# Optimization experiments

Hardware: AMD Instinct MI355X
Metric: run time of the kernel (lower is better)

The kernel has to match this reference:

```python
import jax, jax.numpy as jnp
import numpy as np

N, G, S = 51200, 512, 100   # nodes, graphs, nodes per graph
E = 512000                   # edges (within-graph)
F, H, D = 64, 4, 64
HD = H * D                   # 256
C = 10
RATIO = 0.8
NEG = -1e30


def _seg_softmax(logits, seg, mask, num_seg):
    # masked softmax over edges grouped by destination node
    lg = jnp.where(mask[:, None], logits, NEG)
    m = jax.lax.stop_gradient(jax.ops.segment_max(lg, seg, num_segments=num_seg))
    ex = jnp.where(mask[:, None], jnp.exp(lg - m[seg]), 0.0)
    s = jax.ops.segment_sum(ex, seg, num_segments=num_seg)
    return ex / jnp.maximum(s[seg], 1e-16)


def _gat_conv(x, src, dst, nmask, emask, W, att, b, Wres):
    # PyG GATConv: heads=4, concat=True, add_self_loops=True, residual Linear
    h = (x @ W).reshape(N, H, D)
    a_src = (h * att[0]).sum(-1)   # [N,H]
    a_dst = (h * att[1]).sum(-1)
    loop = jnp.arange(N, dtype=src.dtype)
    s2 = jnp.concatenate([src, loop])
    d2 = jnp.concatenate([dst, loop])
    em2 = jnp.concatenate([emask, nmask])
    logits = jax.nn.leaky_relu(a_src[s2] + a_dst[d2], 0.2)   # [E+N,H]
    alpha = _seg_softmax(logits, d2, em2, N)
    out = jax.ops.segment_sum(h[s2] * alpha[:, :, None], d2, num_segments=N)
    out = out.reshape(N, HD) + x @ Wres + b
    return out * nmask[:, None]


def _gt_conv(x, src, dst, nmask, emask, Wqkv, bqkv, Wskip, bskip):
    # PyG TransformerConv: heads=4, concat=True, root_weight=True (lin_skip)
    qkv = (x @ Wqkv + bqkv).reshape(N, 3, H, D)
    q, k, v = qkv[:, 0], qkv[:, 1], qkv[:, 2]
    logits = (q[dst] * k[src]).sum(-1) * (1.0 / np.sqrt(D))   # [E,H]
    alpha = _seg_softmax(logits, dst, emask, N)
    out = jax.ops.segment_sum(v[src] * alpha[:, :, None], dst, num_segments=N)
    return (out.reshape(N, HD) + x @ Wskip + bskip) * nmask[:, None]


def _topk_pool(x, w, batch, nmask, emask, src, dst):
    # PyG TopKPooling: score=tanh(x.w/|w|), keep top ceil(0.8*n) per graph,
    # x <- x*score, drop edges touching removed nodes. Masked (static-shape) form.
    score = jnp.tanh((x @ w) / jnp.linalg.norm(w))
    keyv = jnp.where(nmask, score, NEG)
    # composite key: sort by graph id, then by score descending (dead nodes last)
    ck = batch.astype(jnp.float32) * 4.0 - jnp.clip(keyv, -1.5, 1.5)
    order = jnp.argsort(ck)
    n_alive = jax.ops.segment_sum(nmask.astype(jnp.int32), batch, num_segments=G)
    k = jnp.ceil(RATIO * n_alive.astype(jnp.float32)).astype(jnp.int32)
    counts = jax.ops.segment_sum(jnp.ones(N, jnp.int32), batch, num_segments=G)
    start = jnp.cumsum(counts) - counts
    gs = batch[order]
    rank = jnp.arange(N, dtype=jnp.int32) - start[gs]
    keep = jnp.zeros(N, bool).at[order].set(rank < k[gs]) & nmask
    x_new = jnp.where(keep[:, None], x * score[:, None], 0.0)
    emask_new = emask & keep[src] & keep[dst]
    return x_new, keep, emask_new


def _readout(x, batch, nmask):
    # torch_geometric gmp || gap over alive nodes
    mx = jax.ops.segment_max(jnp.where(nmask[:, None], x, NEG), batch, num_segments=G)
    sm = jax.ops.segment_sum(x * nmask[:, None].astype(x.dtype), batch, num_segments=G)
    cnt = jax.ops.segment_sum(nmask.astype(x.dtype), batch, num_segments=G)
    return jnp.concatenate([mx, sm / jnp.maximum(cnt, 1.0)[:, None]], axis=1)


def _branch(x, src, dst, batch, conv, layers, pool_w):
    nmask = jnp.ones(N, bool)
    emask = jnp.ones(E, bool)
    acc = jnp.zeros((G, 2 * HD), x.dtype)
    for i in range(3):
        x = jax.nn.relu(conv(x, src, dst, nmask, emask, *layers[i]))
        x, nmask, emask = _topk_pool(x, pool_w[i], batch, nmask, emask, src, dst)
        acc = acc + _readout(x, batch, nmask)
    return acc


def _forward(x, edge_index, batch, gat1_W, gat1_att, gat1_b, gat1_res, gat2_W, gat2_att, gat2_b, gat2_res, gat3_W, gat3_att, gat3_b, gat3_res, gat_pool_w, gt1_Wqkv, gt1_bqkv, gt1_Wskip, gt1_bskip, gt2_Wqkv, gt2_bqkv, gt2_Wskip, gt2_bskip, gt3_Wqkv, gt3_bqkv, gt3_Wskip, gt3_bskip, gt_pool_w, lin1_W, lin1_b, lin2_W, lin2_b, lin3_W, lin3_b):
    src, dst = edge_index[0], edge_index[1]
    gat_layers = [(gat1_W, gat1_att, gat1_b, gat1_res),
                  (gat2_W, gat2_att, gat2_b, gat2_res),
                  (gat3_W, gat3_att, gat3_b, gat3_res)]
    gt_layers = [(gt1_Wqkv, gt1_bqkv, gt1_Wskip, gt1_bskip),
                 (gt2_Wqkv, gt2_bqkv, gt2_Wskip, gt2_bskip),
                 (gt3_Wqkv, gt3_bqkv, gt3_Wskip, gt3_bskip)]
    h1 = _branch(x, src, dst, batch, _gat_conv, gat_layers, gat_pool_w)
    h2 = _branch(x, src, dst, batch, _gt_conv, gt_layers, gt_pool_w)
    h = jnp.concatenate([h1, h2], axis=1)   # [G, 1024]
    h = jax.nn.relu(h @ lin1_W + lin1_b)
    # dropout p=0.5 skipped (eval mode)
    h = jax.nn.relu(h @ lin2_W + lin2_b)
    return jax.nn.log_softmax(h @ lin3_W + lin3_b, axis=-1)


def setup_inputs():
    keys = iter(jax.random.split(jax.random.key(0), 64))
    def nrm(shape, scale):
        return jax.random.normal(next(keys), shape, jnp.float32) * scale
    inp = {}
    inp["x"] = nrm((N, F), 1.0)
    src = jax.random.randint(next(keys), (E,), 0, N, jnp.int32)
    off = jax.random.randint(next(keys), (E,), 0, S, jnp.int32)
    dst = (src // S) * S + off   # keep edges within the source node's graph
    inp["edge_index"] = jnp.stack([src, dst])
    inp["batch"] = jnp.arange(N, dtype=jnp.int32) // S
    ins = [F, HD, HD]
    for i in range(3):
        fi = ins[i]
        sc = 1.0 / np.sqrt(fi)
        inp[f"gat{i+1}_W"] = nrm((fi, HD), sc)
        inp[f"gat{i+1}_att"] = nrm((2, H, D), 0.1)
        inp[f"gat{i+1}_b"] = jnp.zeros((HD,), jnp.float32)
        inp[f"gat{i+1}_res"] = nrm((fi, HD), sc)
        inp[f"gt{i+1}_Wqkv"] = nrm((fi, 3 * HD), sc)
        inp[f"gt{i+1}_bqkv"] = jnp.zeros((3 * HD,), jnp.float32)
        inp[f"gt{i+1}_Wskip"] = nrm((fi, HD), sc)
        inp[f"gt{i+1}_bskip"] = jnp.zeros((HD,), jnp.float32)
    inp["gat_pool_w"] = nrm((3, HD), 0.1)
    inp["gt_pool_w"] = nrm((3, HD), 0.1)
    inp["lin1_W"] = nrm((4 * HD, 128), 1.0 / np.sqrt(4 * HD))
    inp["lin1_b"] = jnp.zeros((128,), jnp.float32)
    inp["lin2_W"] = nrm((128, 64), 1.0 / np.sqrt(128.0))
    inp["lin2_b"] = jnp.zeros((64,), jnp.float32)
    inp["lin3_W"] = nrm((64, C), 1.0 / np.sqrt(64.0))
    inp["lin3_b"] = jnp.zeros((C,), jnp.float32)
    return inp


def reference(x, edge_index, batch, gat1_W, gat1_att, gat1_b, gat1_res, gat2_W, gat2_att, gat2_b, gat2_res, gat3_W, gat3_att, gat3_b, gat3_res, gat_pool_w, gt1_Wqkv, gt1_bqkv, gt1_Wskip, gt1_bskip, gt2_Wqkv, gt2_bqkv, gt2_Wskip, gt2_bskip, gt3_Wqkv, gt3_bqkv, gt3_Wskip, gt3_bskip, gt_pool_w, lin1_W, lin1_b, lin2_W, lin2_b, lin3_W, lin3_b):
    return _forward(x, edge_index, batch, gat1_W, gat1_att, gat1_b, gat1_res, gat2_W, gat2_att, gat2_b, gat2_res, gat3_W, gat3_att, gat3_b, gat3_res, gat_pool_w, gt1_Wqkv, gt1_bqkv, gt1_Wskip, gt1_bskip, gt2_Wqkv, gt2_bqkv, gt2_Wskip, gt2_bskip, gt3_Wqkv, gt3_bqkv, gt3_Wskip, gt3_bskip, gt_pool_w, lin1_W, lin1_b, lin2_W, lin2_b, lin3_W, lin3_b)
```

## Files before the change

kernel.cpp:

```cpp
#include <hip/hip_runtime.h>
#include <hip/hip_bf16.h>
#include <math.h>

#define N_NODES 51200
#define N_GRAPHS 512
#define S_NODES 100
#define N_EDGES 512000
#define HDF 256
#define NEGF (-1e30f)
#define DCAP 128

typedef short bf16x8 __attribute__((ext_vector_type(8)));
typedef float f32x4 __attribute__((ext_vector_type(4)));

__device__ inline unsigned short f2b(float x) {
    union { float f; unsigned u; } v; v.f = x;
    unsigned r = v.u + 0x7FFFu + ((v.u >> 16) & 1u);
    return (unsigned short)(r >> 16);
}
__device__ inline float b2f(unsigned short b) {
    union { float f; unsigned u; } v; v.u = ((unsigned)b) << 16; return v.f;
}

__global__ void set_int(int* __restrict__ p, int v, int n) {
    int i = blockIdx.x * 256 + threadIdx.x;
    if (i < n) p[i] = v;
}

__global__ void init_zero(int* __restrict__ deg, int* __restrict__ cursor,
                          float* __restrict__ acc1, float* __restrict__ acc2) {
    int i = blockIdx.x * 256 + threadIdx.x;
    if (i < N_NODES) { deg[i] = 0; cursor[i] = 0; }
    acc1[i] = 0.f;
    acc2[i] = 0.f;
}

struct WSplitDesc { const float* W; unsigned short* Wh; unsigned short* Wl; int K, NC; };
struct WSplitPack { WSplitDesc d[12]; };
__global__ void wsplit_all(WSplitPack p) {
    WSplitDesc d = p.d[blockIdx.y];
    int idx = blockIdx.x * 256 + threadIdx.x;
    if (idx >= d.K * d.NC) return;
    int k = idx / d.NC, c = idx - k * d.NC;
    float v = d.W[idx];
    unsigned short h = f2b(v);
    int o = ((k >> 3) * d.NC + c) * 8 + (k & 7);
    d.Wh[o] = h;
    d.Wl[o] = f2b(v - b2f(h));
}

__global__ __launch_bounds__(512) void mfma_gemm(
    const float* __restrict__ A,
    const unsigned short* __restrict__ Bh_g, const unsigned short* __restrict__ Bl_g,
    const float* __restrict__ bias, float* __restrict__ C,
    int K, int NC,
    const float* __restrict__ agg, int aggStride,
    const int* __restrict__ nmaskArr,
    const float* __restrict__ rowScale, const int* __restrict__ rsMask)
{
    __shared__ unsigned short Ah[4 * 128 * 8];
    __shared__ unsigned short Al[4 * 128 * 8];
    int row0 = blockIdx.y * 128, col0 = blockIdx.x * 256;
    int t = threadIdx.x;
    int lane = t & 63, w = t >> 6;
    int wr = w >> 2, wc = w & 3;
    int l15 = lane & 15, l4 = lane >> 4;
    f32x4 acc[4][4];
    #pragma unroll
    for (int m = 0; m < 4; ++m)
        #pragma unroll
        for (int n = 0; n < 4; ++n) acc[m][n] = (f32x4){0.f, 0.f, 0.f, 0.f};

    int arow = t & 127, akg = t >> 7;
    float ascale = 1.f;
    if (rowScale) ascale = rsMask[row0 + arow] ? rowScale[row0 + arow] : 0.f;

    for (int k0 = 0; k0 < K; k0 += 32) {
        const float* ap = A + (size_t)(row0 + arow) * K + k0 + akg * 8;
        float4 a0 = *(const float4*)ap;
        float4 a1 = *(const float4*)(ap + 4);
        float av[8] = {a0.x, a0.y, a0.z, a0.w, a1.x, a1.y, a1.z, a1.w};
        int abase = (akg * 128 + arow) * 8;
        #pragma unroll
        for (int j = 0; j < 8; ++j) {
            float s = av[j] * ascale;
            unsigned short h = f2b(s);
            Ah[abase + j] = h;
            Al[abase + j] = f2b(s - b2f(h));
        }
        __syncthreads();
        bf16x8 bh[4], bl[4];
        size_t brow = (size_t)((k0 >> 3) + l4) * NC;
        #pragma unroll
        for (int n = 0; n < 4; ++n) {
            size_t gb = (brow + col0 + wc * 64 + n * 16 + l15) * 8;
            bh[n] = *(const bf16x8*)&Bh_g[gb];
            bl[n] = *(const bf16x8*)&Bl_g[gb];
        }
        #pragma unroll
        for (int m = 0; m < 4; ++m) {
            int idx = (l4 * 128 + wr * 64 + m * 16 + l15) * 8;
            bf16x8 ah = *(bf16x8*)&Ah[idx];
            bf16x8 al = *(bf16x8*)&Al[idx];
            #pragma unroll
            for (int n = 0; n < 4; ++n) {
                acc[m][n] = __builtin_amdgcn_mfma_f32_16x16x32_bf16(ah, bh[n], acc[m][n], 0, 0, 0);
                acc[m][n] = __builtin_amdgcn_mfma_f32_16x16x32_bf16(ah, bl[n], acc[m][n], 0, 0, 0);
                acc[m][n] = __builtin_amdgcn_mfma_f32_16x16x32_bf16(al, bh[n], acc[m][n], 0, 0, 0);
            }
        }
        __syncthreads();
    }
    bool fused = (agg != nullptr);
    #pragma unroll
    for (int m = 0; m < 4; ++m) {
        #pragma unroll
        for (int n = 0; n < 4; ++n) {
            int col = col0 + wc * 64 + n * 16 + l15;
            float bv = bias ? bias[col] : 0.f;
            #pragma unroll
            for (int r = 0; r < 4; ++r) {
                int row = row0 + wr * 64 + m * 16 + l4 * 4 + r;
                float v = acc[m][n][r] + bv;
                if (fused) {
                    v += agg[(size_t)row * aggStride + col];
                    float nm = nmaskArr[row] ? 1.f : 0.f;
                    C[(size_t)row * 256 + col] = fmaxf(v, 0.f) * nm;
                } else {
                    C[(size_t)row * NC + col] = v;
                }
            }
        }
    }
}

__global__ void count_deg(const int* __restrict__ dst, int* __restrict__ deg) {
    int e = blockIdx.x * 256 + threadIdx.x;
    atomicAdd(&deg[dst[e]], 1);
}

__global__ __launch_bounds__(1024) void scan_deg(const int* __restrict__ deg,
                                                 int* __restrict__ rowStart) {
    __shared__ int part[1024];
    int t = threadIdx.x;
    const int chunk = N_NODES / 1024;
    int s = t * chunk;
    int sum = 0;
    for (int i = 0; i < chunk; ++i) sum += deg[s + i];
    part[t] = sum;
    __syncthreads();
    for (int d = 1; d < 1024; d <<= 1) {
        int v = (t >= d) ? part[t - d] : 0;
        __syncthreads();
        part[t] += v;
        __syncthreads();
    }
    int excl = (t == 0) ? 0 : part[t - 1];
    for (int i = 0; i < chunk; ++i) { rowStart[s + i] = excl; excl += deg[s + i]; }
    if (t == 1023) rowStart[N_NODES] = part[1023];
}

__global__ void scatter_edges(const int* __restrict__ src, const int* __restrict__ dst,
                              int* __restrict__ cursor, const int* __restrict__ rowStart,
                              int* __restrict__ csrSrc) {
    int e = blockIdx.x * 256 + threadIdx.x;
    int d = dst[e];
    int p = atomicAdd(&cursor[d], 1);
    csrSrc[rowStart[d] + p] = src[e];
}

__global__ __launch_bounds__(256) void gat_att_pw(const float* __restrict__ hfeat,
                                                  const float* __restrict__ att,
                                                  float* __restrict__ aS,
                                                  float* __restrict__ aD) {
    int t = threadIdx.x, w = t >> 6, l = t & 63;
    int i = blockIdx.x * 4 + w;
    int h = l >> 4, g16 = l & 15;
    float4 hv = *(const float4*)&hfeat[i * HDF + l * 4];
    float4 a0 = *(const float4*)&att[l * 4];
    float4 a1 = *(const float4*)&att[256 + l * 4];
    float p0 = hv.x * a0.x + hv.y * a0.y + hv.z * a0.z + hv.w * a0.w;
    float p1 = hv.x * a1.x + hv.y * a1.y + hv.z * a1.z + hv.w * a1.w;
    p0 += __shfl_xor(p0, 1, 64);  p1 += __shfl_xor(p1, 1, 64);
    p0 += __shfl_xor(p0, 2, 64);  p1 += __shfl_xor(p1, 2, 64);
    p0 += __shfl_xor(p0, 4, 64);  p1 += __shfl_xor(p1, 4, 64);
    p0 += __shfl_xor(p0, 8, 64);  p1 += __shfl_xor(p1, 8, 64);
    if (g16 == 0) { aS[i * 4 + h] = p0; aD[i * 4 + h] = p1; }
}

__global__ __launch_bounds__(256) void gat_edge_pg(
    const float* __restrict__ hfeat, const float* __restrict__ aS, const float* __restrict__ aD,
    const int* __restrict__ rowStart, const int* __restrict__ csrSrc,
    const int* __restrict__ nmask,
    float* __restrict__ aggOut)
{
    int bid = blockIdx.x;
    int t = threadIdx.x, w = t >> 6, l = t & 63;
    int i = (bid & 7) * (N_NODES / 8) + (bid >> 3) * 4 + w;
    int h = l >> 4, g16 = l & 15;
    __shared__ float sL[4][4][DCAP + 8];
    __shared__ int   sS[4][DCAP + 8];
    if (!nmask[i]) {
        *(float4*)&aggOut[i * HDF + l * 4] = make_float4(0.f, 0.f, 0.f, 0.f);
        return;
    }
    int rs = rowStart[i];
    int deg = min(rowStart[i + 1] - rs, DCAP);
    for (int j = l; j < deg; j += 64) {
        int s_ = csrSrc[rs + j];
        sS[w][j] = nmask[s_] ? s_ : -1;
    }
    if (l == 0) sS[w][deg] = i;
    float adh = aD[i * 4 + h];
    for (int j = g16; j < deg; j += 16) {
        int s_ = sS[w][j];
        float lg = NEGF;
        if (s_ >= 0) {
            lg = aS[s_ * 4 + h] + adh;
            lg = (lg >= 0.f) ? lg : 0.2f * lg;
        }
        sL[w][h][j] = lg;
    }
    if (g16 == (deg & 15)) {
        float lg = aS[i * 4 + h] + adh;
        sL[w][h][deg] = (lg >= 0.f) ? lg : 0.2f * lg;
    }
    int tot = deg + 1;
    float m = NEGF;
    for (int j = g16; j < tot; j += 16) m = fmaxf(m, sL[w][h][j]);
    m = fmaxf(m, __shfl_xor(m, 1, 64));
    m = fmaxf(m, __shfl_xor(m, 2, 64));
    m = fmaxf(m, __shfl_xor(m, 4, 64));
    m = fmaxf(m, __shfl_xor(m, 8, 64));
    float sum = 0.f;
    for (int j = g16; j < tot; j += 16) {
        float lv = sL[w][h][j];
        float e = (lv > -1e29f) ? __expf(lv - m) : 0.f;
        sL[w][h][j] = e;
        sum += e;
    }
    sum += __shfl_xor(sum, 1, 64);
    sum += __shfl_xor(sum, 2, 64);
    sum += __shfl_xor(sum, 4, 64);
    sum += __shfl_xor(sum, 8, 64);
    float inv = 1.f / fmaxf(sum, 1e-16f);
    float4 a4 = make_float4(0.f, 0.f, 0.f, 0.f);
    for (int j = 0; j < tot; ++j) {
        int s_ = sS[w][j];
        if (s_ < 0) continue;
        float a = sL[w][h][j] * inv;
        float4 v4 = *(const float4*)&hfeat[s_ * HDF + l * 4];
        a4.x += a * v4.x; a4.y += a * v4.y; a4.z += a * v4.z; a4.w += a * v4.w;
    }
    *(float4*)&aggOut[i * HDF + l * 4] = a4;
}

__global__ __launch_bounds__(256) void gt_edge_pg(
    float* __restrict__ qkv,
    const int* __restrict__ rowStart, const int* __restrict__ csrSrc,
    const int* __restrict__ nmask)
{
    int bid = blockIdx.x;
    int t = threadIdx.x, w = t >> 6, l = t & 63;
    int i = (bid & 7) * (N_NODES / 8) + (bid >> 3) * 4 + w;
    int h = l >> 4, g16 = l & 15;
    __shared__ float sL[4][4][DCAP + 8];
    __shared__ int   sS[4][DCAP + 8];
    if (!nmask[i]) {
        *(float4*)&qkv[i * 768 + l * 4] = make_float4(0.f, 0.f, 0.f, 0.f);
        return;
    }
    int rs = rowStart[i];
    int deg = min(rowStart[i + 1] - rs, DCAP);
    for (int j = l; j < deg; j += 64) {
        int s_ = csrSrc[rs + j];
        sS[w][j] = nmask[s_] ? s_ : -1;
    }
    float4 q4 = *(const float4*)&qkv[i * 768 + l * 4];
    for (int j = 0; j < deg; ++j) {
        int s_ = sS[w][j];
        float p = 0.f;
        if (s_ >= 0) {
            float4 k4 = *(const float4*)&qkv[s_ * 768 + 256 + l * 4];
            p = q4.x * k4.x + q4.y * k4.y + q4.z * k4.z + q4.w * k4.w;
        }
        p += __shfl_xor(p, 1, 64);
        p += __shfl_xor(p, 2, 64);
        p += __shfl_xor(p, 4, 64);
        p += __shfl_xor(p, 8, 64);
        if (g16 == 0) sL[w][h][j] = (s_ >= 0) ? p * 0.125f : NEGF;
    }
    float m = NEGF;
    for (int j = g16; j < deg; j += 16) m = fmaxf(m, sL[w][h][j]);
    m = fmaxf(m, __shfl_xor(m, 1, 64));
    m = fmaxf(m, __shfl_xor(m, 2, 64));
    m = fmaxf(m, __shfl_xor(m, 4, 64));
    m = fmaxf(m, __shfl_xor(m, 8, 64));
    float sum = 0.f;
    for (int j = g16; j < deg; j += 16) {
        float lv = sL[w][h][j];
        float e = (lv > -1e29f) ? __expf(lv - m) : 0.f;
        sL[w][h][j] = e;
        sum += e;
    }
    sum += __shfl_xor(sum, 1, 64);
    sum += __shfl_xor(sum, 2, 64);
    sum += __shfl_xor(sum, 4, 64);
    sum += __shfl_xor(sum, 8, 64);
    float inv = 1.f / fmaxf(sum, 1e-16f);
    float4 a4 = make_float4(0.f, 0.f, 0.f, 0.f);
    for (int j = 0; j < deg; ++j) {
        int s_ = sS[w][j];
        if (s_ < 0) continue;
        float a = sL[w][h][j] * inv;
        float4 v4 = *(const float4*)&qkv[s_ * 768 + 512 + l * 4];
        a4.x += a * v4.x; a4.y += a * v4.y; a4.z += a * v4.z; a4.w += a * v4.w;
    }
    *(float4*)&qkv[i * 768 + l * 4] = a4;
}

__global__ __launch_bounds__(256) void spr_kernel(
    const float* __restrict__ x, const float* __restrict__ w,
    float* __restrict__ score, int* __restrict__ nmask, float* __restrict__ acc)
{
    int g = blockIdx.x, t = threadIdx.x;
    int wv = t >> 6, l = t & 63;
    __shared__ float sW[256];
    __shared__ float sRaw[104];
    __shared__ float sFin[104];
    __shared__ int   sKeep[104];
    __shared__ float swn;
    __shared__ int cnt_s;
    if (t == 0) cnt_s = 0;
    sW[t] = w[t];
    __syncthreads();
    if (wv == 0) {
        float dw = 0.f;
        #pragma unroll
        for (int c = 0; c < 4; ++c) { float v = sW[l + c * 64]; dw += v * v; }
        #pragma unroll
        for (int o = 32; o > 0; o >>= 1) dw += __shfl_down(dw, o, 64);
        if (l == 0) swn = sqrtf(dw);
    }
    int base = g * S_NODES;
    for (int u = 0; u < 25; ++u) {
        int nl = wv * 25 + u;
        float dx = 0.f;
        #pragma unroll
        for (int c = 0; c < 4; ++c) {
            int cc = l + c * 64;
            dx += x[(size_t)(base + nl) * HDF + cc] * sW[cc];
        }
        #pragma unroll
        for (int o = 32; o > 0; o >>= 1) dx += __shfl_down(dx, o, 64);
        if (l == 0) sRaw[nl] = dx;
    }
    __syncthreads();
    int alive = 0;
    float ck = -2.0f;
    if (t < S_NODES) {
        float sc = tanhf(sRaw[t] / swn);
        sFin[t] = sc;
        score[base + t] = sc;
        alive = nmask[base + t];
        ck = alive ? sc : -1.5f;
        sRaw[t] = ck;
        if (alive) atomicAdd(&cnt_s, 1);
    }
    __syncthreads();
    int k = (int)ceilf(0.8f * (float)cnt_s);
    if (t < S_NODES) {
        int rank = 0;
        for (int jj = 0; jj < S_NODES; ++jj) {
            float o = sRaw[jj];
            rank += (o > ck || (o == ck && jj < t)) ? 1 : 0;
        }
        int kp = (alive && rank < k) ? 1 : 0;
        sKeep[t] = kp;
        nmask[base + t] = kp;
    }
    __syncthreads();
    float mx = NEGF, sm = 0.f, cnt = 0.f;
    for (int o = 0; o < S_NODES; o += 4) {
        float v0 = x[(size_t)(base + o + 0) * HDF + t];
        float v1 = x[(size_t)(base + o + 1) * HDF + t];
        float v2 = x[(size_t)(base + o + 2) * HDF + t];
        float v3 = x[(size_t)(base + o + 3) * HDF + t];
        if (sKeep[o + 0]) { float v = v0 * sFin[o + 0]; mx = fmaxf(mx, v); sm += v; cnt += 1.f; }
        if (sKeep[o + 1]) { float v = v1 * sFin[o + 1]; mx = fmaxf(mx, v); sm += v; cnt += 1.f; }
        if (sKeep[o + 2]) { float v = v2 * sFin[o + 2]; mx = fmaxf(mx, v); sm += v; cnt += 1.f; }
        if (sKeep[o + 3]) { float v = v3 * sFin[o + 3]; mx = fmaxf(mx, v); sm += v; cnt += 1.f; }
    }
    acc[(size_t)g * 512 + t] += mx;
    acc[(size_t)g * 512 + 256 + t] += sm / fmaxf(cnt, 1.f);
}

__global__ __launch_bounds__(128) void mlp_kernel(
    const float* __restrict__ acc1, const float* __restrict__ acc2,
    const float* __restrict__ W1, const float* __restrict__ b1,
    const float* __restrict__ W2, const float* __restrict__ b2,
    const float* __restrict__ W3, const float* __restrict__ b3,
    float* __restrict__ out)
{
    int g = blockIdx.x, t = threadIdx.x;
    __shared__ float hrow[1024];
    __shared__ float h1s[128];
    __shared__ float h2s[64];
    __shared__ float o3[10];
    for (int j = t; j < 512; j += 128) {
        hrow[j] = acc1[(size_t)g * 512 + j];
        hrow[512 + j] = acc2[(size_t)g * 512 + j];
    }
    __syncthreads();
    float s = b1[t];
    for (int kx = 0; kx < 1024; ++kx) s += hrow[kx] * W1[(size_t)kx * 128 + t];
    h1s[t] = fmaxf(s, 0.f);
    __syncthreads();
    if (t < 64) {
        float s2 = b2[t];
        for (int kx = 0; kx < 128; ++kx) s2 += h1s[kx] * W2[kx * 64 + t];
        h2s[t] = fmaxf(s2, 0.f);
    }
    __syncthreads();
    if (t < 10) {
        float s3 = b3[t];
        for (int kx = 0; kx < 64; ++kx) s3 += h2s[kx] * W3[kx * 10 + t];
        o3[t] = s3;
    }
    __syncthreads();
    if (t < 10) {
        float m = o3[0];
        for (int j = 1; j < 10; ++j) m = fmaxf(m, o3[j]);
        float se = 0.f;
        for (int j = 0; j < 10; ++j) se += expf(o3[j] - m);
        out[g * 10 + t] = o3[t] - m - logf(se);
    }
}

extern "C" void kernel_launch(void* const* d_in, const int* in_sizes, int n_in,
                              void* d_out, int out_size, void* d_ws, size_t ws_size,
                              hipStream_t stream) {
    (void)n_in; (void)out_size; (void)ws_size;
    const float* x0 = (const float*)d_in[0];
    const int* src = (const int*)d_in[1];
    const int* dst = src + N_EDGES;

    bool dictOrder = (in_sizes[7] == 64 * 768);
    const float *gatW[3], *gatAtt[3], *gatB[3], *gatRes[3];
    const float *gtWqkv[3], *gtBqkv[3], *gtWskip[3], *gtBskip[3];
    const float *gatPool, *gtPool;
    if (dictOrder) {
        for (int l = 0; l < 3; ++l) {
            int b = 3 + l * 8;
            gatW[l]    = (const float*)d_in[b + 0];
            gatAtt[l]  = (const float*)d_in[b + 1];
            gatB[l]    = (const float*)d_in[b + 2];
            gatRes[l]  = (const float*)d_in[b + 3];
            gtWqkv[l]  = (const float*)d_in[b + 4];
            gtBqkv[l]  = (const float*)d_in[b + 5];
            gtWskip[l] = (const float*)d_in[b + 6];
            gtBskip[l] = (const float*)d_in[b + 7];
        }
        gatPool = (const float*)d_in[27];
        gtPool  = (const float*)d_in[28];
    } else {
        for (int l = 0; l < 3; ++l) {
            int b = 3 + l * 4;
            gatW[l]   = (const float*)d_in[b + 0];
            gatAtt[l] = (const float*)d_in[b + 1];
            gatB[l]   = (const float*)d_in[b + 2];
            gatRes[l] = (const float*)d_in[b + 3];
            int c = 16 + l * 4;
            gtWqkv[l]  = (const float*)d_in[c + 0];
            gtBqkv[l]  = (const float*)d_in[c + 1];
            gtWskip[l] = (const float*)d_in[c + 2];
            gtBskip[l] = (const float*)d_in[c + 3];
        }
        gatPool = (const float*)d_in[15];
        gtPool  = (const float*)d_in[28];
    }
    const float* lin1W = (const float*)d_in[29];
    const float* lin1b = (const float*)d_in[30];
    const float* lin2W = (const float*)d_in[31];
    const float* lin2b = (const float*)d_in[32];
    const float* lin3W = (const float*)d_in[33];
    const float* lin3b = (const float*)d_in[34];

    char* wsp = (char*)d_ws;
    size_t off = 0;
    auto carve = [&](size_t bytes) -> void* {
        void* p = wsp + off;
        off += (bytes + 255) & ~(size_t)255;
        return p;
    };
    float* bufX   = (float*)carve((size_t)N_NODES * HDF * 4);
    float* bufH   = (float*)carve((size_t)N_NODES * 768 * 4);
    float* aS     = (float*)carve((size_t)N_NODES * 4 * 4);
    float* aD     = (float*)carve((size_t)N_NODES * 4 * 4);
    float* scoreB = (float*)carve((size_t)N_NODES * 4);
    int* nmask    = (int*)carve((size_t)N_NODES * 4);
    int* deg      = (int*)carve((size_t)N_NODES * 4);
    int* rowStart = (int*)carve((size_t)(N_NODES + 1) * 4);
    int* cursor   = (int*)carve((size_t)N_NODES * 4);
    int* csrSrc   = (int*)carve((size_t)N_EDGES * 4);
    float* acc1   = (float*)carve((size_t)N_GRAPHS * 512 * 4);
    float* acc2   = (float*)carve((size_t)N_GRAPHS * 512 * 4);
    const int wElems = 884736;
    unsigned short* whBase = (unsigned short*)carve((size_t)wElems * 2);
    unsigned short* wlBase = (unsigned short*)carve((size_t)wElems * 2);
    float* ysec   = bufH + (size_t)N_NODES * HDF;

    unsigned short *WH[12], *WL[12];
    {
        WSplitPack pack;
        int o = 0, maxSz = 0;
        for (int l = 0; l < 3; ++l) {
            int fi = (l == 0) ? 64 : 256;
            int sz[4] = {fi * 256, fi * 256, fi * 768, fi * 256};
            const float* Wp[4] = {gatW[l], gatRes[l], gtWqkv[l], gtWskip[l]};
            int NCs[4] = {256, 256, 768, 256};
            for (int q = 0; q < 4; ++q) {
                int idx = l * 4 + q;
                WH[idx] = whBase + o;
                WL[idx] = wlBase + o;
                pack.d[idx] = {Wp[q], WH[idx], WL[idx], fi, NCs[q]};
                if (sz[q] > maxSz) maxSz = sz[q];
                o += sz[q];
            }
        }
        wsplit_all<<<dim3((maxSz + 255) / 256, 12), 256, 0, stream>>>(pack);
    }

    init_zero<<<(N_GRAPHS * 512) / 256, 256, 0, stream>>>(deg, cursor, acc1, acc2);
    count_deg<<<N_EDGES / 256, 256, 0, stream>>>(dst, deg);
    scan_deg<<<1, 1024, 0, stream>>>(deg, rowStart);
    scatter_edges<<<N_EDGES / 256, 256, 0, stream>>>(src, dst, cursor, rowStart, csrSrc);

    for (int br = 0; br < 2; ++br) {
        bool isGAT = (br == 0);
        float* acc = isGAT ? acc1 : acc2;
        const float* poolW = isGAT ? gatPool : gtPool;
        set_int<<<N_NODES / 256, 256, 0, stream>>>(nmask, 1, N_NODES);
        const float* xcur = x0;
        int fi = 64;
        for (int l = 0; l < 3; ++l) {
            const float* rs = (l == 0) ? nullptr : scoreB;
            const int* rsm = (l == 0) ? nullptr : nmask;
            if (isGAT) {
                mfma_gemm<<<dim3(1, N_NODES / 128), 512, 0, stream>>>(
                    xcur, WH[l * 4 + 0], WL[l * 4 + 0], nullptr, bufH, fi, 256,
                    nullptr, 0, nullptr, rs, rsm);
                gat_att_pw<<<N_NODES / 4, 256, 0, stream>>>(bufH, gatAtt[l], aS, aD);
                gat_edge_pg<<<N_NODES / 4, 256, 0, stream>>>(bufH, aS, aD, rowStart,
                                                             csrSrc, nmask, ysec);
                mfma_gemm<<<dim3(1, N_NODES / 128), 512, 0, stream>>>(
                    xcur, WH[l * 4 + 1], WL[l * 4 + 1], gatB[l], bufX, fi, 256,
                    ysec, HDF, nmask, rs, rsm);
            } else {
                mfma_gemm<<<dim3(3, N_NODES / 128), 512, 0, stream>>>(
                    xcur, WH[l * 4 + 2], WL[l * 4 + 2], gtBqkv[l], bufH, fi, 768,
                    nullptr, 0, nullptr, rs, rsm);
                gt_edge_pg<<<N_NODES / 4, 256, 0, stream>>>(bufH, rowStart, csrSrc,
                                                            nmask);
                mfma_gemm<<<dim3(1, N_NODES / 128), 512, 0, stream>>>(
                    xcur, WH[l * 4 + 3], WL[l * 4 + 3], gtBskip[l], bufX, fi, 256,
                    bufH , 768, nmask, rs, rsm);
            }
            spr_kernel<<<N_GRAPHS, 256, 0, stream>>>(bufX, poolW + l * HDF,
                                                     scoreB, nmask, acc);
            xcur = bufX;
            fi = HDF;
        }
    }
    mlp_kernel<<<N_GRAPHS, 128, 0, stream>>>(acc1, acc2, lin1W, lin1b, lin2W, lin2b,
                                             lin3W, lin3b, (float*)d_out);
}
```

Before: 1.222 ms.

## Store activations pre-split into bf16 hi/lo in a k-blocked layout

Activations are now kept as split bf16 hi/lo pairs in a k-grouped layout, written directly by the fused GEMM epilogue. The GEMMs then load A fragments straight from global memory instead of converting fp32 into LDS each k-step, which drops the LDS staging and both barriers per step. The TopK row scaling moves from the A load into the output epilogue, which is valid because scaling a row commutes with the matmul. The cost is that the pooling kernel must read the strided split layout, giving poorer coalescing, and the fused GEMM overwrites its own input buffer in place. That in-place write is safe only because each block reads and writes the same row range, with a barrier in between.

```diff
diff --git a/kernel.cpp b/kernel.cpp
--- a/kernel.cpp
+++ b/kernel.cpp
@@ -49,20 +49,26 @@
     d.Wl[o] = f2b(v - b2f(h));
 }
 
-__global__ __launch_bounds__(512) void mfma_gemm(
-    const float* __restrict__ A,
-    const unsigned short* __restrict__ Bh_g, const unsigned short* __restrict__ Bl_g,
+__global__ void asplit64(const float* __restrict__ X,
+                         unsigned short* __restrict__ Xh, unsigned short* __restrict__ Xl) {
+    int idx = blockIdx.x * 256 + threadIdx.x;
+    int row = idx >> 6, k = idx & 63;
+    float v = X[idx];
+    unsigned short h = f2b(v);
+    int o = ((k >> 3) * N_NODES + row) * 8 + (k & 7);
+    Xh[o] = h;
+    Xl[o] = f2b(v - b2f(h));
+}
+
+__global__ __launch_bounds__(512) void gemm_main(
+    const unsigned short* __restrict__ Ah, const unsigned short* __restrict__ Al,
+    const unsigned short* __restrict__ Bh, const unsigned short* __restrict__ Bl,
     const float* __restrict__ bias, float* __restrict__ C,
     int K, int NC,
-    const float* __restrict__ agg, int aggStride,
-    const int* __restrict__ nmaskArr,
     const float* __restrict__ rowScale, const int* __restrict__ rsMask)
 {
-    __shared__ unsigned short Ah[4 * 128 * 8];
-    __shared__ unsigned short Al[4 * 128 * 8];
     int row0 = blockIdx.y * 128, col0 = blockIdx.x * 256;
-    int t = threadIdx.x;
-    int lane = t & 63, w = t >> 6;
+    int t = threadIdx.x, lane = t & 63, w = t >> 6;
     int wr = w >> 2, wc = w & 3;
     int l15 = lane & 15, l4 = lane >> 4;
     f32x4 acc[4][4];
@@ -71,64 +77,120 @@
         #pragma unroll
         for (int n = 0; n < 4; ++n) acc[m][n] = (f32x4){0.f, 0.f, 0.f, 0.f};
 
-    int arow = t & 127, akg = t >> 7;
-    float ascale = 1.f;
-    if (rowScale) ascale = rsMask[row0 + arow] ? rowScale[row0 + arow] : 0.f;
-
     for (int k0 = 0; k0 < K; k0 += 32) {
-        const float* ap = A + (size_t)(row0 + arow) * K + k0 + akg * 8;
-        float4 a0 = *(const float4*)ap;
-        float4 a1 = *(const float4*)(ap + 4);
-        float av[8] = {a0.x, a0.y, a0.z, a0.w, a1.x, a1.y, a1.z, a1.w};
-        int abase = (akg * 128 + arow) * 8;
-        #pragma unroll
-        for (int j = 0; j < 8; ++j) {
-            float s = av[j] * ascale;
-            unsigned short h = f2b(s);
-            Ah[abase + j] = h;
-            Al[abase + j] = f2b(s - b2f(h));
-        }
-        __syncthreads();
-        bf16x8 bh[4], bl[4];
-        size_t brow = (size_t)((k0 >> 3) + l4) * NC;
+        int kg = (k0 >> 3) + l4;
+        size_t arow = (size_t)kg * N_NODES;
+        size_t brow = (size_t)kg * NC;
+        bf16x8 ah[4], al[4], bh[4], bl[4];
         #pragma unroll
         for (int n = 0; n < 4; ++n) {
             size_t gb = (brow + col0 + wc * 64 + n * 16 + l15) * 8;
-            bh[n] = *(const bf16x8*)&Bh_g[gb];
-            bl[n] = *(const bf16x8*)&Bl_g[gb];
+            bh[n] = *(const bf16x8*)&Bh[gb];
+            bl[n] = *(const bf16x8*)&Bl[gb];
         }
         #pragma unroll
         for (int m = 0; m < 4; ++m) {
-            int idx = (l4 * 128 + wr * 64 + m * 16 + l15) * 8;
-            bf16x8 ah = *(bf16x8*)&Ah[idx];
-            bf16x8 al = *(bf16x8*)&Al[idx];
+            size_t ga = (arow + row0 + wr * 64 + m * 16 + l15) * 8;
+            ah[m] = *(const bf16x8*)&Ah[ga];
+            al[m] = *(const bf16x8*)&Al[ga];
+        }
+        #pragma unroll
+        for (int m = 0; m < 4; ++m)
             #pragma unroll
             for (int n = 0; n < 4; ++n) {
-                acc[m][n] = __builtin_amdgcn_mfma_f32_16x16x32_bf16(ah, bh[n], acc[m][n], 0, 0, 0);
-                acc[m][n] = __builtin_amdgcn_mfma_f32_16x16x32_bf16(ah, bl[n], acc[m][n], 0, 0, 0);
-                acc[m][n] = __builtin_amdgcn_mfma_f32_16x16x32_bf16(al, bh[n], acc[m][n], 0, 0, 0);
+                acc[m][n] = __builtin_amdgcn_mfma_f32_16x16x32_bf16(ah[m], bh[n], acc[m][n], 0, 0, 0);
+                acc[m][n] = __builtin_amdgcn_mfma_f32_16x16x32_bf16(ah[m], bl[n], acc[m][n], 0, 0, 0);
+                acc[m][n] = __builtin_amdgcn_mfma_f32_16x16x32_bf16(al[m], bh[n], acc[m][n], 0, 0, 0);
             }
-        }
-        __syncthreads();
-    }
-    bool fused = (agg != nullptr);
+    }
     #pragma unroll
     for (int m = 0; m < 4; ++m) {
+        int rbase = row0 + wr * 64 + m * 16 + l4 * 4;
+        float sr[4];
+        #pragma unroll
+        for (int r = 0; r < 4; ++r)
+            sr[r] = rowScale ? (rsMask[rbase + r] ? rowScale[rbase + r] : 0.f) : 1.f;
         #pragma unroll
         for (int n = 0; n < 4; ++n) {
             int col = col0 + wc * 64 + n * 16 + l15;
             float bv = bias ? bias[col] : 0.f;
             #pragma unroll
+            for (int r = 0; r < 4; ++r)
+                C[(size_t)(rbase + r) * NC + col] = sr[r] * acc[m][n][r] + bv;
+        }
+    }
+}
+
+__global__ __launch_bounds__(512) void gemm_fused(
+    const unsigned short* __restrict__ Ah, const unsigned short* __restrict__ Al,
+    const unsigned short* __restrict__ Bh, const unsigned short* __restrict__ Bl,
+    const float* __restrict__ bias,
+    const float* __restrict__ agg, int aggStride,
+    const int* __restrict__ nmaskArr,
+    int K,
+    const float* __restrict__ rowScale, const int* __restrict__ rsMask,
+    unsigned short* __restrict__ Xh, unsigned short* __restrict__ Xl)
+{
+    const int NC = 256;
+    int row0 = blockIdx.y * 128;
+    int t = threadIdx.x, lane = t & 63, w = t >> 6;
+    int wr = w >> 2, wc = w & 3;
+    int l15 = lane & 15, l4 = lane >> 4;
+    f32x4 acc[4][4];
+    #pragma unroll
+    for (int m = 0; m < 4; ++m)
+        #pragma unroll
+        for (int n = 0; n < 4; ++n) acc[m][n] = (f32x4){0.f, 0.f, 0.f, 0.f};
+
+    for (int k0 = 0; k0 < K; k0 += 32) {
+        int kg = (k0 >> 3) + l4;
+        size_t arow = (size_t)kg * N_NODES;
+        size_t brow = (size_t)kg * NC;
+        bf16x8 ah[4], al[4], bh[4], bl[4];
+        #pragma unroll
+        for (int n = 0; n < 4; ++n) {
+            size_t gb = (brow + wc * 64 + n * 16 + l15) * 8;
+            bh[n] = *(const bf16x8*)&Bh[gb];
+            bl[n] = *(const bf16x8*)&Bl[gb];
+        }
+        #pragma unroll
+        for (int m = 0; m < 4; ++m) {
+            size_t ga = (arow + row0 + wr * 64 + m * 16 + l15) * 8;
+            ah[m] = *(const bf16x8*)&Ah[ga];
+            al[m] = *(const bf16x8*)&Al[ga];
+        }
+        #pragma unroll
+        for (int m = 0; m < 4; ++m)
+            #pragma unroll
+            for (int n = 0; n < 4; ++n) {
+                acc[m][n] = __builtin_amdgcn_mfma_f32_16x16x32_bf16(ah[m], bh[n], acc[m][n], 0, 0, 0);
+                acc[m][n] = __builtin_amdgcn_mfma_f32_16x16x32_bf16(ah[m], bl[n], acc[m][n], 0, 0, 0);
+                acc[m][n] = __builtin_amdgcn_mfma_f32_16x16x32_bf16(al[m], bh[n], acc[m][n], 0, 0, 0);
+            }
+    }
+    __syncthreads();
+    #pragma unroll
+    for (int m = 0; m < 4; ++m) {
+        int rbase = row0 + wr * 64 + m * 16 + l4 * 4;
+        float sr[4], nm[4];
+        #pragma unroll
+        for (int r = 0; r < 4; ++r) {
+            sr[r] = rowScale ? (rsMask[rbase + r] ? rowScale[rbase + r] : 0.f) : 1.f;
+            nm[r] = nmaskArr[rbase + r] ? 1.f : 0.f;
+        }
+        #pragma unroll
+        for (int n = 0; n < 4; ++n) {
+            int col = wc * 64 + n * 16 + l15;
+            float bv = bias[col];
+            int obase = ((col >> 3) * N_NODES) * 8 + (col & 7);
+            #pragma unroll
             for (int r = 0; r < 4; ++r) {
-                int row = row0 + wr * 64 + m * 16 + l4 * 4 + r;
-                float v = acc[m][n][r] + bv;
-                if (fused) {
-                    v += agg[(size_t)row * aggStride + col];
-                    float nm = nmaskArr[row] ? 1.f : 0.f;
-                    C[(size_t)row * 256 + col] = fmaxf(v, 0.f) * nm;
-                } else {
-                    C[(size_t)row * NC + col] = v;
-                }
+                int row = rbase + r;
+                float v = fmaxf(sr[r] * acc[m][n][r] + agg[(size_t)row * aggStride + col] + bv, 0.f) * nm[r];
+                int o = obase + row * 8;
+                unsigned short h = f2b(v);
+                Xh[o] = h;
+                Xl[o] = f2b(v - b2f(h));
             }
         }
     }
@@ -320,7 +382,8 @@
 }
 
 __global__ __launch_bounds__(256) void spr_kernel(
-    const float* __restrict__ x, const float* __restrict__ w,
+    const unsigned short* __restrict__ Xh, const unsigned short* __restrict__ Xl,
+    const float* __restrict__ w,
     float* __restrict__ score, int* __restrict__ nmask, float* __restrict__ acc)
 {
     int g = blockIdx.x, t = threadIdx.x;
@@ -345,11 +408,14 @@
     int base = g * S_NODES;
     for (int u = 0; u < 25; ++u) {
         int nl = wv * 25 + u;
+        int row = base + nl;
         float dx = 0.f;
         #pragma unroll
         for (int c = 0; c < 4; ++c) {
             int cc = l + c * 64;
-            dx += x[(size_t)(base + nl) * HDF + cc] * sW[cc];
+            int a = ((cc >> 3) * N_NODES + row) * 8 + (cc & 7);
+            float xv = b2f(Xh[a]) + b2f(Xl[a]);
+            dx += xv * sW[cc];
         }
         #pragma unroll
         for (int o = 32; o > 0; o >>= 1) dx += __shfl_down(dx, o, 64);
@@ -380,12 +446,17 @@
         nmask[base + t] = kp;
     }
     __syncthreads();
+    int tbase = ((t >> 3) * N_NODES) * 8 + (t & 7);
     float mx = NEGF, sm = 0.f, cnt = 0.f;
     for (int o = 0; o < S_NODES; o += 4) {
-        float v0 = x[(size_t)(base + o + 0) * HDF + t];
-        float v1 = x[(size_t)(base + o + 1) * HDF + t];
-        float v2 = x[(size_t)(base + o + 2) * HDF + t];
-        float v3 = x[(size_t)(base + o + 3) * HDF + t];
+        int a0 = tbase + (base + o + 0) * 8;
+        int a1 = tbase + (base + o + 1) * 8;
+        int a2 = tbase + (base + o + 2) * 8;
+        int a3 = tbase + (base + o + 3) * 8;
+        float v0 = b2f(Xh[a0]) + b2f(Xl[a0]);
+        float v1 = b2f(Xh[a1]) + b2f(Xl[a1]);
+        float v2 = b2f(Xh[a2]) + b2f(Xl[a2]);
+        float v3 = b2f(Xh[a3]) + b2f(Xl[a3]);
         if (sKeep[o + 0]) { float v = v0 * sFin[o + 0]; mx = fmaxf(mx, v); sm += v; cnt += 1.f; }
         if (sKeep[o + 1]) { float v = v1 * sFin[o + 1]; mx = fmaxf(mx, v); sm += v; cnt += 1.f; }
         if (sKeep[o + 2]) { float v = v2 * sFin[o + 2]; mx = fmaxf(mx, v); sm += v; cnt += 1.f; }
@@ -493,8 +564,9 @@
         off += (bytes + 255) & ~(size_t)255;
         return p;
     };
-    float* bufX   = (float*)carve((size_t)N_NODES * HDF * 4);
     float* bufH   = (float*)carve((size_t)N_NODES * 768 * 4);
+    unsigned short* Xh = (unsigned short*)carve((size_t)N_NODES * 256 * 2);
+    unsigned short* Xl = (unsigned short*)carve((size_t)N_NODES * 256 * 2);
     float* aS     = (float*)carve((size_t)N_NODES * 4 * 4);
     float* aD     = (float*)carve((size_t)N_NODES * 4 * 4);
     float* scoreB = (float*)carve((size_t)N_NODES * 4);
@@ -541,34 +613,30 @@
         float* acc = isGAT ? acc1 : acc2;
         const float* poolW = isGAT ? gatPool : gtPool;
         set_int<<<N_NODES / 256, 256, 0, stream>>>(nmask, 1, N_NODES);
-        const float* xcur = x0;
+        asplit64<<<(N_NODES * 64) / 256, 256, 0, stream>>>(x0, Xh, Xl);
         int fi = 64;
         for (int l = 0; l < 3; ++l) {
             const float* rs = (l == 0) ? nullptr : scoreB;
             const int* rsm = (l == 0) ? nullptr : nmask;
             if (isGAT) {
-                mfma_gemm<<<dim3(1, N_NODES / 128), 512, 0, stream>>>(
-                    xcur, WH[l * 4 + 0], WL[l * 4 + 0], nullptr, bufH, fi, 256,
-                    nullptr, 0, nullptr, rs, rsm);
+                gemm_main<<<dim3(1, N_NODES / 128), 512, 0, stream>>>(
+                    Xh, Xl, WH[l * 4 + 0], WL[l * 4 + 0], nullptr, bufH, fi, 256, rs, rsm);
                 gat_att_pw<<<N_NODES / 4, 256, 0, stream>>>(bufH, gatAtt[l], aS, aD);
                 gat_edge_pg<<<N_NODES / 4, 256, 0, stream>>>(bufH, aS, aD, rowStart,
                                                              csrSrc, nmask, ysec);
-                mfma_gemm<<<dim3(1, N_NODES / 128), 512, 0, stream>>>(
-                    xcur, WH[l * 4 + 1], WL[l * 4 + 1], gatB[l], bufX, fi, 256,
-                    ysec, HDF, nmask, rs, rsm);
+                gemm_fused<<<dim3(1, N_NODES / 128), 512, 0, stream>>>(
+                    Xh, Xl, WH[l * 4 + 1], WL[l * 4 + 1], gatB[l], ysec, HDF,
+                    nmask, fi, rs, rsm, Xh, Xl);
             } else {
-                mfma_gemm<<<dim3(3, N_NODES / 128), 512, 0, stream>>>(
-                    xcur, WH[l * 4 + 2], WL[l * 4 + 2], gtBqkv[l], bufH, fi, 768,
-                    nullptr, 0, nullptr, rs, rsm);
-                gt_edge_pg<<<N_NODES / 4, 256, 0, stream>>>(bufH, rowStart, csrSrc,
-                                                            nmask);
-                mfma_gemm<<<dim3(1, N_NODES / 128), 512, 0, stream>>>(
-                    xcur, WH[l * 4 + 3], WL[l * 4 + 3], gtBskip[l], bufX, fi, 256,
-                    bufH , 768, nmask, rs, rsm);
+                gemm_main<<<dim3(3, N_NODES / 128), 512, 0, stream>>>(
+                    Xh, Xl, WH[l * 4 + 2], WL[l * 4 + 2], gtBqkv[l], bufH, fi, 768, rs, rsm);
+                gt_edge_pg<<<N_NODES / 4, 256, 0, stream>>>(bufH, rowStart, csrSrc, nmask);
+                gemm_fused<<<dim3(1, N_NODES / 128), 512, 0, stream>>>(
+                    Xh, Xl, WH[l * 4 + 3], WL[l * 4 + 3], gtBskip[l], bufH , 768,
+                    nmask, fi, rs, rsm, Xh, Xl);
             }
-            spr_kernel<<<N_GRAPHS, 256, 0, stream>>>(bufX, poolW + l * HDF,
+            spr_kernel<<<N_GRAPHS, 256, 0, stream>>>(Xh, Xl, poolW + l * HDF,
                                                      scoreB, nmask, acc);
-            xcur = bufX;
             fi = HDF;
         }
     }
```

Result: slower. 1.412 ms, median of 4 (+15.6%).
